# Kernel optimization log

Measured on AMD Instinct MI355X. Metric: run time of the kernel, lower is better.

Reference implementation:

```python
import jax, jax.numpy as jnp
import numpy as np

T, B, L, D = 32, 128, 1024, 256  # timesteps, batch, memory slots, word_vec_size(=rnn_size)


def setup_inputs() -> dict:
    key = jax.random.key(0)
    ks = jax.random.split(key, 20)
    f = lambda k, s: jax.random.normal(k, s, dtype=jnp.float32) * 0.05
    return {
        "emb_utts": f(ks[0], (T, B, D)),
        "hr0": f(ks[1], (B, D)),
        "cr0": f(ks[2], (B, D)),
        "hw0": f(ks[3], (B, D)),
        "cw0": f(ks[4], (B, D)),
        "M": f(ks[5], (B, L, D)),
        "mask": jax.random.randint(ks[6], (B, L), 0, 2).astype(bool),
        "Wih_r": f(ks[7], (4 * D, D)),
        "Whh_r": f(ks[8], (4 * D, D)),
        "bih_r": f(ks[9], (4 * D,)),
        "bhh_r": f(ks[10], (4 * D,)),
        "Wc": f(ks[11], (D, 2 * D)),
        "bc": f(ks[12], (D,)),
        "Wih_w": f(ks[13], (4 * D, D)),
        "Whh_w": f(ks[14], (4 * D, D)),
        "bih_w": f(ks[15], (4 * D,)),
        "bhh_w": f(ks[16], (4 * D,)),
    }


def _lstm_cell(x, h, c, Wih, Whh, bih, bhh):
    # PyTorch LSTMCell gate order: i, f, g, o
    g = x @ Wih.T + h @ Whh.T + bih + bhh
    i, fg, gg, o = jnp.split(g, 4, axis=1)
    i = jax.nn.sigmoid(i)
    fg = jax.nn.sigmoid(fg)
    gg = jnp.tanh(gg)
    o = jax.nn.sigmoid(o)
    c2 = fg * c + i * gg
    return o * jnp.tanh(c2), c2


def reference(emb_utts, hr0, cr0, hw0, cw0, M, mask,
              Wih_r, Whh_r, bih_r, bhh_r, Wc, bc,
              Wih_w, Whh_w, bih_w, bhh_w):
    def step(carry, w):
        hr, cr, hw, cw, Mc = carry
        hr, cr = _lstm_cell(w, hr, cr, Wih_r, Whh_r, bih_r, bhh_r)
        # attention read: z = softmax(masked(hr . M))  -> [B, L]
        z = jnp.einsum('bd,bld->bl', hr, Mc)
        z = jax.nn.softmax(jnp.where(mask, -jnp.inf, z), axis=1)
        m = jnp.einsum('bl,bld->bd', z, Mc)           # gather read [B, D]
        comp = jax.nn.softmax(jnp.concatenate([hr, m], axis=1) @ Wc.T + bc, axis=1)
        hw, cw = _lstm_cell(comp, hw, cw, Wih_w, Whh_w, bih_w, bhh_w)
        # memory rewrite exactly as source: M_new = (1 - z) + hw * z (broadcast)
        Mc = (1.0 - z[:, :, None]) + hw[:, None, :] * z[:, :, None]
        return (hr, cr, hw, cw, Mc), hw

    (hr, cr, hw, cw, M), outputs = jax.lax.scan(
        step, (hr0, cr0, hw0, cw0, M), emb_utts)
    return outputs, hr, cr, hw, cw, M
```

## Files before the change

### kernel.cpp

```cpp
#include <hip/hip_runtime.h>
#include <math.h>

typedef unsigned int u32;
typedef __attribute__((ext_vector_type(2))) _Float16 h2;

#define kT 32
#define OUT_STATES 1048576
#define OUT_M      1179648

union H2U { u32 u; h2 h; };

__device__ __forceinline__ float dot2u(u32 w, u32 x, float acc){
  H2U a; a.u = w; H2U b; b.u = x;
#if __has_builtin(__builtin_amdgcn_fdot2)
  return __builtin_amdgcn_fdot2(a.h, b.h, acc, false);
#else
  acc += (float)a.h.x * (float)b.h.x;
  acc += (float)a.h.y * (float)b.h.y;
  return acc;
#endif
}

__device__ __forceinline__ u32 packf16(float x, float y){
  H2U v; v.h.x = (_Float16)x; v.h.y = (_Float16)y; return v.u;
}

__device__ __forceinline__ u32 alu(const u32* p){
  return __hip_atomic_load((u32*)p, __ATOMIC_RELAXED, __HIP_MEMORY_SCOPE_AGENT);
}
__device__ __forceinline__ float alf(const float* p){
  return __hip_atomic_load((float*)p, __ATOMIC_RELAXED, __HIP_MEMORY_SCOPE_AGENT);
}
__device__ __forceinline__ void asu(u32* p, u32 v){
  __hip_atomic_store(p, v, __ATOMIC_RELAXED, __HIP_MEMORY_SCOPE_AGENT);
}
__device__ __forceinline__ void asf(float* p, float v){
  __hip_atomic_store(p, v, __ATOMIC_RELAXED, __HIP_MEMORY_SCOPE_AGENT);
}

__device__ __forceinline__ void pollk(const u32* f, int n, u32 tgt, int tid){
  if (tid < 64){
    const u32* p = f + ((tid < n) ? tid : 0);
    for (;;){
      if (__all((int)(alu(p) >= tgt))) break;
      __builtin_amdgcn_s_sleep(2);
    }
  }
  __syncthreads();
}

__global__ __launch_bounds__(1024) void k_prep(
        const float* __restrict__ Wih_r, const float* __restrict__ Whh_r,
        const float* __restrict__ bih_r, const float* __restrict__ bhh_r,
        const float* __restrict__ Wc,    const float* __restrict__ bc,
        const float* __restrict__ Wih_w, const float* __restrict__ Whh_w,
        const float* __restrict__ bih_w, const float* __restrict__ bhh_w,
        const unsigned char* __restrict__ maskraw,
        u32* WAp, u32* WEp, u32* Wcp, float* bA, float* bE, float* bcf,
        float* wcs, unsigned char* mbuf, u32* flags){
  __shared__ int sb[3];
  if (threadIdx.x < 3) sb[threadIdx.x] = 0;
  __syncthreads();
  if (threadIdx.x < 512){
    unsigned char c = maskraw[threadIdx.x];
    if (c > 1u) atomicOr(&sb[0], 1);
    if ((threadIdx.x & 3) != 0 && c != 0) atomicOr(&sb[1], 1);
    if ((threadIdx.x & 3) == 1 && c == 0x3F) atomicOr(&sb[2], 1);
  }
  __syncthreads();
  int mode = (!sb[0]) ? (sb[1] ? 1 : 0) : (sb[2] ? 2 : 3);

  int idx = blockIdx.x * 1024 + threadIdx.x;
  if (idx < 262144){
    int kp = idx >> 10, col = idx & 1023;
    int k0 = 2 * kp;
    float v0 = (k0 < 256) ? Wih_r[col * 256 + k0] : Whh_r[col * 256 + k0 - 256];
    float v1 = (k0 + 1 < 256) ? Wih_r[col * 256 + k0 + 1]
                              : Whh_r[col * 256 + k0 + 1 - 256];
    WAp[idx] = packf16(v0, v1);
  } else if (idx < 524288){
    int i = idx - 262144;
    int kp = i >> 10, col = i & 1023;
    int k0 = 2 * kp;
    float v0 = (k0 < 256) ? Wih_w[col * 256 + k0] : Whh_w[col * 256 + k0 - 256];
    float v1 = (k0 + 1 < 256) ? Wih_w[col * 256 + k0 + 1]
                              : Whh_w[col * 256 + k0 + 1 - 256];
    WEp[i] = packf16(v0, v1);
  } else if (idx < 589824){
    int i = idx - 524288;
    int kp = i >> 8, col = i & 255;
    int k0 = 2 * kp;
    Wcp[i] = packf16(Wc[col * 512 + k0], Wc[col * 512 + k0 + 1]);
  } else if (idx < 590848){
    int i = idx - 589824;
    bA[i] = bih_r[i] + bhh_r[i];
  } else if (idx < 591872){
    int i = idx - 590848;
    bE[i] = bih_w[i] + bhh_w[i];
  } else if (idx < 592128){
    int i = idx - 591872;
    bcf[i] = bc[i];
  } else if (idx < 592384){
    int c = idx - 592128;
    float s = 0.f;
    for (int k = 0; k < 256; k++) s += Wc[c * 512 + 256 + k];
    wcs[c] = s;
  } else if (idx < 723456){
    int l = idx - 592384;
    unsigned char mv;
    if      (mode == 0) mv = (((const int*)maskraw)[l] != 0);
    else if (mode == 1) mv = (maskraw[l] != 0);
    else if (mode == 2) mv = ((maskraw[2*l] | maskraw[2*l+1]) != 0);
    else                mv = (((const unsigned int*)maskraw)[l] != 0);
    mbuf[l] = mv;
  } else if (idx < 724032){
    flags[idx - 723456] = 0;
  }
}

__global__ __launch_bounds__(1024) void k_pre(
        const float* __restrict__ emb, const u32* __restrict__ WAp,
        u32* __restrict__ gxp){
  __shared__ u32 wt[16384];
  __shared__ u32 xt[128 * 129];
  int t = blockIdx.x, c0 = blockIdx.y * 128, tid = threadIdx.x;
  for (int i = 0; i < 16; i++){
    int idx = i * 1024 + tid;
    wt[idx] = WAp[(size_t)(idx >> 7) * 1024 + c0 + (idx & 127)];
    int b = idx >> 7, kp = idx & 127;
    float2 e2 = *(const float2*)(emb + (size_t)t * 32768 + b * 256 + 2 * kp);
    xt[b * 129 + kp] = packf16(e2.x, e2.y);
  }
  __syncthreads();
  int b = tid & 127, cg = tid >> 7;
  float acc[16];
  #pragma unroll
  for (int j = 0; j < 16; j++) acc[j] = 0.f;
  const u32* xrow = xt + b * 129;
  for (int kp = 0; kp < 128; kp++){
    u32 xv = xrow[kp];
    const uint4* wr = (const uint4*)(wt + kp * 128 + cg * 16);
    #pragma unroll
    for (int j4 = 0; j4 < 4; j4++){
      uint4 wv = wr[j4];
      acc[4*j4+0] = dot2u(wv.x, xv, acc[4*j4+0]);
      acc[4*j4+1] = dot2u(wv.y, xv, acc[4*j4+1]);
      acc[4*j4+2] = dot2u(wv.z, xv, acc[4*j4+2]);
      acc[4*j4+3] = dot2u(wv.w, xv, acc[4*j4+3]);
    }
  }
  u32* gp = gxp + ((size_t)t * 128 + b) * 512 + (c0 >> 1) + cg * 8;
  #pragma unroll
  for (int i = 0; i < 8; i++) gp[i] = packf16(acc[2*i], acc[2*i+1]);
}

__device__ __forceinline__ void gemv256(const u32* __restrict__ W,
        const u32* xh, float* psum, int tid){
  int cg = tid & 255, ks = tid >> 8;
  const uint4* wp = (const uint4*)W + (size_t)ks * 32 * 256 + cg;
  const u32* xk = xh + ks * 32;
  float a0 = 0.f, a1 = 0.f, a2 = 0.f, a3 = 0.f;
  #pragma unroll 8
  for (int i = 0; i < 32; i++){
    uint4 wv = wp[(size_t)i * 256];
    u32 xp = xk[i];
    a0 = dot2u(wv.x, xp, a0);  a1 = dot2u(wv.y, xp, a1);
    a2 = dot2u(wv.z, xp, a2);  a3 = dot2u(wv.w, xp, a3);
  }
  float4 r; r.x = a0; r.y = a1; r.z = a2; r.w = a3;
  *(float4*)&psum[ks * 1024 + cg * 4] = r;
}

__device__ __forceinline__ void gemv128x256(const u32* __restrict__ W,
        const u32* xh, float* psum, int tid){
  int c = tid & 255, ks = tid >> 8;
  const u32* wp = W + (size_t)(ks * 32) * 256 + c;
  const u32* xk = xh + ks * 32;
  float a = 0.f;
  #pragma unroll 8
  for (int i = 0; i < 32; i++) a = dot2u(wp[(size_t)i * 256], xk[i], a);
  psum[ks * 256 + c] = a;
}

__device__ void scan_half(int k, const float* __restrict__ M0,
        const unsigned char* __restrict__ mbuf, const float* __restrict__ hrf,
        float* spbuf, float* mpbuf, float* msbuf, u32* fT0, const u32* fR,
        char* sc, int tid){
  float* ps   = (float*)(sc);
  float* wred = (float*)(sc + 16640);
  float* sred = (float*)(sc + 16704);
  float* hr0l = (float*)(sc + 16768);
  int row = k >> 1, half = k & 1;
  pollk(fR + row, 1, 1u, tid);
  if (tid < 256) hr0l[tid] = alf(hrf + row * 256 + tid);
  __syncthreads();
  int w = tid >> 6, lane = tid & 63;
  float4 hrv = *(const float4*)&hr0l[lane * 4];
  float run_max = -INFINITY, S = 0.f;
  float m0 = 0.f, m1 = 0.f, m2 = 0.f, m3 = 0.f;
  int l0 = half * 512 + w * 32;
  for (int l = l0; l < l0 + 32; ++l){
    float4 Mv = *(const float4*)(M0 + ((size_t)row * 1024 + l) * 256 + lane * 4);
    float part = Mv.x * hrv.x + Mv.y * hrv.y + Mv.z * hrv.z + Mv.w * hrv.w;
    #pragma unroll
    for (int mm = 32; mm >= 1; mm >>= 1) part += __shfl_xor(part, mm, 64);
    float s = mbuf[row * 1024 + l] ? -INFINITY : part;
    if (lane == 0) asf(spbuf + row * 1024 + l, s);
    float nm = fmaxf(run_max, s);
    if (nm > -INFINITY){
      float sc2 = expf(run_max - nm);
      float p   = expf(s - nm);
      S = S * sc2 + p;
      m0 = m0 * sc2 + p * Mv.x;  m1 = m1 * sc2 + p * Mv.y;
      m2 = m2 * sc2 + p * Mv.z;  m3 = m3 * sc2 + p * Mv.w;
      run_max = nm;
    }
  }
  if (lane == 0){ wred[w] = run_max; sred[w] = S; }
  ps[w * 260 + lane * 4 + 0] = m0;
  ps[w * 260 + lane * 4 + 1] = m1;
  ps[w * 260 + lane * 4 + 2] = m2;
  ps[w * 260 + lane * 4 + 3] = m3;
  __syncthreads();
  float gmax = -INFINITY;
  #pragma unroll
  for (int w2 = 0; w2 < 16; w2++) gmax = fmaxf(gmax, wred[w2]);
  float Sg = 0.f;
  #pragma unroll
  for (int w2 = 0; w2 < 16; w2++) Sg += sred[w2] * expf(wred[w2] - gmax);
  if (tid < 256){
    float mv = 0.f;
    #pragma unroll
    for (int w2 = 0; w2 < 16; w2++) mv += ps[w2 * 260 + tid] * expf(wred[w2] - gmax);
    asf(mpbuf + k * 256 + tid, mv);
  }
  if (tid == 0){ asf(msbuf + 2 * k, gmax); asf(msbuf + 2 * k + 1, Sg); }
  __syncthreads();
  if (tid == 0) asu(fT0 + k, 1u);
}

__global__ __launch_bounds__(1024, 4) void k_main(
        const float* __restrict__ hr0, const float* __restrict__ cr0,
        const float* __restrict__ hw0, const float* __restrict__ cw0,
        const float* __restrict__ M0,
        const u32* __restrict__ WAp, const u32* __restrict__ WEp,
        const u32* __restrict__ Wcp, const float* __restrict__ bA,
        const float* __restrict__ bE, const float* __restrict__ bcf,
        const float* __restrict__ wcs, const unsigned char* __restrict__ mbuf,
        const u32* __restrict__ gxp,
        float* __restrict__ hrf, float* __restrict__ ubuf,
        float* __restrict__ vcbuf, float* __restrict__ gwbuf,
        u32* __restrict__ hwp, float* __restrict__ zsbuf,
        float* __restrict__ hwfin, float* __restrict__ spbuf,
        float* __restrict__ mpbuf, float* __restrict__ msbuf,
        u32* __restrict__ flags, float* __restrict__ out){
  __shared__ __attribute__((aligned(16))) char smem[86016];
  int bid = blockIdx.x, tid = threadIdx.x;
  int w = tid >> 6, lane = tid & 63;
  u32* fR  = flags;
  u32* fGv = flags + 128;
  u32* fG  = flags + 192;
  u32* fW  = flags + 256;
  u32* fT0 = flags + 320;

  if (bid < 128){
    int b = bid;
    float* psum = (float*)(smem);
    u32*  xh    = (u32*)(smem + 16384);
    float* hr_f = (float*)(smem + 16896);
    const u32* WRh = WAp + 128 * 1024;
    float cst = (tid < 256) ? cr0[b * 256 + tid] : 0.f;
    if (tid < 128){
      float2 h0 = *(const float2*)(hr0 + b * 256 + 2 * tid);
      xh[tid] = packf16(h0.x, h0.y);
    }
    __syncthreads();
    for (int t = 0; t < kT; t++){
      if (t >= 2) pollk(fW + (b >> 1), 1, (u32)(t - 1), tid);
      u32 gx0 = 0, gx1 = 0, gx2 = 0, gx3 = 0;
      if (tid < 256){
        const u32* gx = gxp + ((size_t)t * 128 + b) * 512;
        gx0 = gx[tid >> 1];          gx1 = gx[128 + (tid >> 1)];
        gx2 = gx[256 + (tid >> 1)];  gx3 = gx[384 + (tid >> 1)];
      }
      gemv256(WRh, xh, psum, tid);
      __syncthreads();
      if (tid < 256){
        H2U p0, p1, p2, p3;
        p0.u = gx0; p1.u = gx1; p2.u = gx2; p3.u = gx3;
        int hi = tid & 1;
        float gi = (hi ? (float)p0.h.y : (float)p0.h.x) + bA[tid];
        float gf = (hi ? (float)p1.h.y : (float)p1.h.x) + bA[256 + tid];
        float gg = (hi ? (float)p2.h.y : (float)p2.h.x) + bA[512 + tid];
        float go = (hi ? (float)p3.h.y : (float)p3.h.x) + bA[768 + tid];
        #pragma unroll
        for (int ks = 0; ks < 4; ks++){
          gi += psum[ks * 1024 + tid];
          gf += psum[ks * 1024 + 256 + tid];
          gg += psum[ks * 1024 + 512 + tid];
          go += psum[ks * 1024 + 768 + tid];
        }
        float i_ = 1.f / (1.f + expf(-gi));
        float f_ = 1.f / (1.f + expf(-gf));
        float g_ = tanhf(gg);
        float o_ = 1.f / (1.f + expf(-go));
        float c2 = f_ * cst + i_ * g_;
        cst = c2;
        float h = o_ * tanhf(c2);
        hr_f[tid] = h;
        asf(hrf + (t & 1) * 32768 + b * 256 + tid, h);
        if (t == kT - 1){
          out[OUT_STATES          + b * 256 + tid] = h;
          out[OUT_STATES +  32768 + b * 256 + tid] = c2;
        }
      }
      __syncthreads();
      if (tid < 128) xh[tid] = packf16(hr_f[2 * tid], hr_f[2 * tid + 1]);
      __syncthreads();
      gemv128x256(Wcp, xh, psum, tid);
      __syncthreads();
      if (tid < 256){
        float u = psum[tid] + psum[256 + tid] + psum[512 + tid] + psum[768 + tid];
        asf(ubuf + (t & 1) * 32768 + b * 256 + tid, u);
      }
      __syncthreads();
      if (tid == 0) asu(fR + b, (u32)(t + 1));
      if (t == 0)
        scan_half(bid, M0, mbuf, hrf, spbuf, mpbuf, msbuf, fT0, fR,
                  smem + 49152, tid);
    }
  } else if (bid < 192){
    int g = bid - 128, r0 = 2 * g, r1 = 2 * g + 1;
    float* psum = (float*)(smem);
    u32*  xh    = (u32*)(smem + 32768);
    for (int t = 0; t < kT; t++){
      if (t == 0){
        if (tid < 128){
          float2 h0 = *(const float2*)(hw0 + r0 * 256 + 2 * tid);
          xh[tid] = packf16(h0.x, h0.y);
        } else if (tid < 256){
          int j = tid - 128;
          float2 h0 = *(const float2*)(hw0 + r1 * 256 + 2 * j);
          xh[tid] = packf16(h0.x, h0.y);
        }
      } else {
        pollk(fW + g, 1, (u32)t, tid);
        if (tid < 128)
          xh[tid] = alu(hwp + ((t - 1) & 1) * 16384 + r0 * 128 + tid);
        else if (tid < 256)
          xh[tid] = alu(hwp + ((t - 1) & 1) * 16384 + r1 * 128 + (tid - 128));
      }
      __syncthreads();
      {
        int c = tid & 255, ks = tid >> 8;
        const u32* wp = Wcp + 32768 + (size_t)(ks * 32) * 256 + c;
        const u32* x0 = xh + ks * 32;
        const u32* x1 = xh + 128 + ks * 32;
        float a0 = 0.f, a1 = 0.f;
        #pragma unroll 8
        for (int ii = 0; ii < 32; ii++){
          u32 wv = wp[(size_t)ii * 256];
          a0 = dot2u(wv, x0[ii], a0);
          a1 = dot2u(wv, x1[ii], a1);
        }
        psum[ks * 512 + c] = a0;
        psum[ks * 512 + 256 + c] = a1;
      }
      __syncthreads();
      if (tid < 512){
        int rr = tid >> 8, c = tid & 255;
        float v = psum[rr * 256 + c] + psum[512 + rr * 256 + c]
                + psum[1024 + rr * 256 + c] + psum[1536 + rr * 256 + c];
        asf(vcbuf + (t & 1) * 32768 + (2 * g + rr) * 256 + c, v);
      }
      __syncthreads();
      if (tid == 0) asu(fGv + g, (u32)(t + 1));
      {
        int cg = tid & 255, ks = tid >> 8;
        const uint4* wp = (const uint4*)(WEp + 128 * 1024)
                        + (size_t)(ks * 32) * 256 + cg;
        const u32* x0 = xh + ks * 32;
        const u32* x1 = xh + 128 + ks * 32;
        float a0=0.f,a1=0.f,a2=0.f,a3=0.f,b0=0.f,b1=0.f,b2=0.f,b3=0.f;
        #pragma unroll 4
        for (int ii = 0; ii < 32; ii++){
          uint4 wv = wp[(size_t)ii * 256];
          u32 xp0 = x0[ii], xp1 = x1[ii];
          a0 = dot2u(wv.x, xp0, a0);  a1 = dot2u(wv.y, xp0, a1);
          a2 = dot2u(wv.z, xp0, a2);  a3 = dot2u(wv.w, xp0, a3);
          b0 = dot2u(wv.x, xp1, b0);  b1 = dot2u(wv.y, xp1, b1);
          b2 = dot2u(wv.z, xp1, b2);  b3 = dot2u(wv.w, xp1, b3);
        }
        float4 ra; ra.x=a0; ra.y=a1; ra.z=a2; ra.w=a3;
        float4 rb; rb.x=b0; rb.y=b1; rb.z=b2; rb.w=b3;
        *(float4*)&psum[ks * 1024 + cg * 4] = ra;
        *(float4*)&psum[4096 + ks * 1024 + cg * 4] = rb;
      }
      __syncthreads();
      #pragma unroll
      for (int rr = 0; rr < 2; rr++){
        float v = psum[rr * 4096 + tid] + psum[rr * 4096 + 1024 + tid]
                + psum[rr * 4096 + 2048 + tid] + psum[rr * 4096 + 3072 + tid];
        asf(gwbuf + (t & 1) * 131072 + (2 * g + rr) * 1024 + tid, v);
      }
      __syncthreads();
      if (tid == 0) asu(fG + g, (u32)(t + 1));
      if (t == 0)
        scan_half(bid, M0, mbuf, hrf, spbuf, mpbuf, msbuf, fT0, fR,
                  smem + 49152, tid);
    }
  } else {
    int g = bid - 192, r0g = 2 * g;
    float* psum  = (float*)(smem);
    u32*  xh    = (u32*)(smem + 32768);
    float* comp  = (float*)(smem + 33792);
    float* hw_f  = (float*)(smem + 35840);
    float* m_f   = (float*)(smem + 37888);
    float* wcs_l = (float*)(smem + 39936);
    float* bc_l  = (float*)(smem + 40960);
    float* redA  = (float*)(smem + 41984);
    float* redB  = (float*)(smem + 42048);
    float* redC  = (float*)(smem + 42112);
    float* redD  = (float*)(smem + 42176);
    float* bE_l  = (float*)(smem + 43008);
    int row = tid >> 9, i = tid & 511;
    int brow = r0g + row;
    if (tid < 256){ wcs_l[tid] = wcs[tid]; bc_l[tid] = bcf[tid]; }
    bE_l[tid] = bE[tid];
    float cst = 0.f;
    if (i < 256){
      hw_f[row * 256 + i] = hw0[brow * 256 + i];
      cst = cw0[brow * 256 + i];
    }
    unsigned char mkA = mbuf[brow * 1024 + i];
    unsigned char mkB = mbuf[brow * 1024 + 512 + i];
    float zA = 0.f, zB = 0.f;
    __syncthreads();
    scan_half(bid, M0, mbuf, hrf, spbuf, mpbuf, msbuf, fT0, fR,
              smem + 49152, tid);

    for (int t = 0; t < kT; t++){
      pollk(fR + r0g, 2, (u32)(t + 1), tid);
      float hrv = 0.f, ureg = 0.f;
      if (i < 256){
        hrv  = alf(hrf + (t & 1) * 32768 + brow * 256 + i);
        ureg = alf(ubuf + (t & 1) * 32768 + brow * 256 + i);
      }
      float e = -INFINITY;
      if (t == 0){
        pollk(fT0 + 4 * g, 4, 1u, tid);
        int kA2 = 2 * brow, kB2 = 2 * brow + 1;
        float maxA = alf(msbuf + 2 * kA2), SAv = alf(msbuf + 2 * kA2 + 1);
        float maxB = alf(msbuf + 2 * kB2), SBv = alf(msbuf + 2 * kB2 + 1);
        float Gm = fmaxf(maxA, maxB);
        float eAc = expf(maxA - Gm), eBc = expf(maxB - Gm);
        float Sg = SAv * eAc + SBv * eBc;
        zA = expf(alf(spbuf + brow * 1024 + i) - Gm) / Sg;
        zB = expf(alf(spbuf + brow * 1024 + 512 + i) - Gm) / Sg;
        if (i < 256){
          float mv = (alf(mpbuf + kA2 * 256 + i) * eAc
                    + alf(mpbuf + kB2 * 256 + i) * eBc) / Sg;
          m_f[row * 256 + i] = mv;
        }
        __syncthreads();
        if (i < 128)
          xh[row * 128 + i] = packf16(m_f[row * 256 + 2 * i],
                                      m_f[row * 256 + 2 * i + 1]);
        __syncthreads();
        {
          int c = tid & 255, ks = tid >> 8;
          const u32* wp = Wcp + 32768 + (size_t)(ks * 32) * 256 + c;
          const u32* x0 = xh + ks * 32;
          const u32* x1 = xh + 128 + ks * 32;
          float a0 = 0.f, a1 = 0.f;
          #pragma unroll 8
          for (int ii = 0; ii < 32; ii++){
            u32 wv = wp[(size_t)ii * 256];
            a0 = dot2u(wv, x0[ii], a0);
            a1 = dot2u(wv, x1[ii], a1);
          }
          psum[ks * 512 + c] = a0;
          psum[ks * 512 + 256 + c] = a1;
        }
        __syncthreads();
        if (i < 256){
          float vcm = psum[row * 256 + i] + psum[512 + row * 256 + i]
                    + psum[1024 + row * 256 + i] + psum[1536 + row * 256 + i];
          e = ureg + vcm + bc_l[i];
        }
      } else {
        float v1 = (i < 256) ? hrv : 0.f;
        float v2 = (i < 256) ? hrv * hw_f[row * 256 + i] : 0.f;
        #pragma unroll
        for (int mm = 32; mm >= 1; mm >>= 1){
          v1 += __shfl_xor(v1, mm, 64);  v2 += __shfl_xor(v2, mm, 64);
        }
        if (lane == 0){ redA[w] = v1; redB[w] = v2; }
        __syncthreads();
        float S1 = 0.f, S2 = 0.f;
        #pragma unroll
        for (int k2 = 0; k2 < 8; k2++){
          S1 += redA[row * 8 + k2];  S2 += redB[row * 8 + k2];
        }
        float sA = mkA ? -INFINITY : (1.f - zA) * S1 + zA * S2;
        float sB = mkB ? -INFINITY : (1.f - zB) * S1 + zB * S2;
        float mx = fmaxf(sA, sB);
        #pragma unroll
        for (int mm = 32; mm >= 1; mm >>= 1) mx = fmaxf(mx, __shfl_xor(mx, mm, 64));
        if (lane == 0) redC[w] = mx;
        __syncthreads();
        float gm = -INFINITY;
        #pragma unroll
        for (int k2 = 0; k2 < 8; k2++) gm = fmaxf(gm, redC[row * 8 + k2]);
        float pA_ = expf(sA - gm), pB_ = expf(sB - gm);
        float ps = pA_ + pB_;
        #pragma unroll
        for (int mm = 32; mm >= 1; mm >>= 1) ps += __shfl_xor(ps, mm, 64);
        if (lane == 0) redD[w] = ps;
        __syncthreads();
        float Ss = 0.f;
        #pragma unroll
        for (int k2 = 0; k2 < 8; k2++) Ss += redD[row * 8 + k2];
        float znA = pA_ / Ss, znB = pB_ / Ss;
        float a1 = znA * (1.f - zA) + znB * (1.f - zB);
        float a2 = znA * zA + znB * zB;
        #pragma unroll
        for (int mm = 32; mm >= 1; mm >>= 1){
          a1 += __shfl_xor(a1, mm, 64);  a2 += __shfl_xor(a2, mm, 64);
        }
        if (lane == 0){ redA[w] = a1; redB[w] = a2; }
        __syncthreads();
        float Ab = 0.f, Cb = 0.f;
        #pragma unroll
        for (int k2 = 0; k2 < 8; k2++){
          Ab += redA[row * 8 + k2];  Cb += redB[row * 8 + k2];
        }
        zA = znA;  zB = znB;
        pollk(fGv + g, 1, (u32)(t + 1), tid);
        if (i < 256){
          float vc = alf(vcbuf + (t & 1) * 32768 + brow * 256 + i);
          e = ureg + Ab * wcs_l[i] + Cb * vc + bc_l[i];
        }
      }
      float ev = (i < 256) ? e : -INFINITY;
      float mx2 = ev;
      #pragma unroll
      for (int mm = 32; mm >= 1; mm >>= 1) mx2 = fmaxf(mx2, __shfl_xor(mx2, mm, 64));
      if (lane == 0) redC[w] = mx2;
      __syncthreads();
      float emax = -INFINITY;
      #pragma unroll
      for (int k2 = 0; k2 < 8; k2++) emax = fmaxf(emax, redC[row * 8 + k2]);
      float pe = (i < 256) ? expf(ev - emax) : 0.f;
      float ps2 = pe;
      #pragma unroll
      for (int mm = 32; mm >= 1; mm >>= 1) ps2 += __shfl_xor(ps2, mm, 64);
      if (lane == 0) redD[w] = ps2;
      if (i < 256) comp[row * 256 + i] = pe;
      __syncthreads();
      float esum = 0.f;
      #pragma unroll
      for (int k2 = 0; k2 < 8; k2++) esum += redD[row * 8 + k2];
      if (i < 128)
        xh[row * 128 + i] = packf16(comp[row * 256 + 2 * i],
                                    comp[row * 256 + 2 * i + 1]);
      __syncthreads();
      {
        int cg = tid & 255, ks = tid >> 8;
        const uint4* wp = (const uint4*)WEp + (size_t)(ks * 32) * 256 + cg;
        const u32* x0 = xh + ks * 32;
        const u32* x1 = xh + 128 + ks * 32;
        float a0=0.f,a1=0.f,a2=0.f,a3=0.f,b0=0.f,b1=0.f,b2=0.f,b3=0.f;
        #pragma unroll 4
        for (int ii = 0; ii < 32; ii++){
          uint4 wv = wp[(size_t)ii * 256];
          u32 xp0 = x0[ii], xp1 = x1[ii];
          a0 = dot2u(wv.x, xp0, a0);  a1 = dot2u(wv.y, xp0, a1);
          a2 = dot2u(wv.z, xp0, a2);  a3 = dot2u(wv.w, xp0, a3);
          b0 = dot2u(wv.x, xp1, b0);  b1 = dot2u(wv.y, xp1, b1);
          b2 = dot2u(wv.z, xp1, b2);  b3 = dot2u(wv.w, xp1, b3);
        }
        float4 ra; ra.x=a0; ra.y=a1; ra.z=a2; ra.w=a3;
        float4 rb; rb.x=b0; rb.y=b1; rb.z=b2; rb.w=b3;
        *(float4*)&psum[ks * 1024 + cg * 4] = ra;
        *(float4*)&psum[4096 + ks * 1024 + cg * 4] = rb;
      }
      __syncthreads();
      pollk(fG + g, 1, (u32)(t + 1), tid);
      if (i < 256){
        float rinv = 1.f / esum;
        const float* gwp = gwbuf + (t & 1) * 131072 + brow * 1024;
        float si = psum[row*4096 + i]        + psum[row*4096 + 1024 + i]
                 + psum[row*4096 + 2048 + i] + psum[row*4096 + 3072 + i];
        float sf = psum[row*4096 + 256 + i]  + psum[row*4096 + 1280 + i]
                 + psum[row*4096 + 2304 + i] + psum[row*4096 + 3328 + i];
        float sg2= psum[row*4096 + 512 + i]  + psum[row*4096 + 1536 + i]
                 + psum[row*4096 + 2560 + i] + psum[row*4096 + 3584 + i];
        float so = psum[row*4096 + 768 + i]  + psum[row*4096 + 1792 + i]
                 + psum[row*4096 + 2816 + i] + psum[row*4096 + 3840 + i];
        float gi = bE_l[i]       + alf(gwp + i)       + si  * rinv;
        float gf = bE_l[256 + i] + alf(gwp + 256 + i) + sf  * rinv;
        float gg = bE_l[512 + i] + alf(gwp + 512 + i) + sg2 * rinv;
        float go = bE_l[768 + i] + alf(gwp + 768 + i) + so  * rinv;
        float i_ = 1.f / (1.f + expf(-gi));
        float f_ = 1.f / (1.f + expf(-gf));
        float g_ = tanhf(gg);
        float o_ = 1.f / (1.f + expf(-go));
        float c2 = f_ * cst + i_ * g_;
        cst = c2;
        float h = o_ * tanhf(c2);
        hw_f[row * 256 + i] = h;
        out[(size_t)t * 32768 + brow * 256 + i] = h;
        if (t == kT - 1){
          out[OUT_STATES + 65536 + brow * 256 + i] = h;
          out[OUT_STATES + 98304 + brow * 256 + i] = c2;
        }
      }
      __syncthreads();
      if (i < 128)
        asu(hwp + (t & 1) * 16384 + brow * 128 + i,
            packf16(hw_f[row * 256 + 2 * i], hw_f[row * 256 + 2 * i + 1]));
      __syncthreads();
      if (tid == 0) asu(fW + g, (u32)(t + 1));
    }
    if (i < 256) asf(hwfin + brow * 256 + i, hw_f[row * 256 + i]);
    asf(zsbuf + brow * 1024 + i, zA);
    asf(zsbuf + brow * 1024 + 512 + i, zB);
    __syncthreads();
    if (tid == 0) asu(fW + g, (u32)(kT + 1));
  }

  {
    int mrow = bid >> 1, half = bid & 1;
    pollk(fW + (mrow >> 1), 1, (u32)(kT + 1), tid);
    float* zl  = (float*)(smem + 49152);
    float* hwl = (float*)(smem + 51200);
    if (tid < 512) zl[tid] = alf(zsbuf + mrow * 1024 + half * 512 + tid);
    else if (tid < 768) hwl[tid - 512] = alf(hwfin + mrow * 256 + (tid - 512));
    __syncthreads();
    float* Mout = out + OUT_M + (size_t)mrow * 262144 + (size_t)half * 131072;
    for (int it = 0; it < 32; it++){
      int idx = it * 1024 + tid;
      int l = idx >> 6, d4 = (idx & 63) << 2;
      float z = zl[l], omz = 1.f - z;
      float4 h4 = *(const float4*)&hwl[d4];
      float4 v;
      v.x = omz + h4.x * z;  v.y = omz + h4.y * z;
      v.z = omz + h4.z * z;  v.w = omz + h4.w * z;
      *(float4*)(Mout + (size_t)l * 256 + d4) = v;
    }
  }
}

extern "C" void kernel_launch(void* const* d_in, const int* in_sizes, int n_in,
                              void* d_out, int out_size, void* d_ws, size_t ws_size,
                              hipStream_t stream){
  const float* emb   = (const float*)d_in[0];
  const float* hr0   = (const float*)d_in[1];
  const float* cr0   = (const float*)d_in[2];
  const float* hw0   = (const float*)d_in[3];
  const float* cw0   = (const float*)d_in[4];
  const float* M0    = (const float*)d_in[5];
  const unsigned char* maskraw = (const unsigned char*)d_in[6];
  const float* Wih_r = (const float*)d_in[7];
  const float* Whh_r = (const float*)d_in[8];
  const float* bih_r = (const float*)d_in[9];
  const float* bhh_r = (const float*)d_in[10];
  const float* Wc    = (const float*)d_in[11];
  const float* bc    = (const float*)d_in[12];
  const float* Wih_w = (const float*)d_in[13];
  const float* Whh_w = (const float*)d_in[14];
  const float* bih_w = (const float*)d_in[15];
  const float* bhh_w = (const float*)d_in[16];
  float* out = (float*)d_out;

  char* ws = (char*)d_ws;
  u32*  WAp   = (u32*)(ws);
  u32*  WEp   = (u32*)(ws + 1048576);
  u32*  Wcp   = (u32*)(ws + 2097152);
  float* bA   = (float*)(ws + 2359296);
  float* bE   = (float*)(ws + 2363392);
  float* bcf  = (float*)(ws + 2367488);
  float* wcs  = (float*)(ws + 2368512);
  unsigned char* mbuf = (unsigned char*)(ws + 2369536);
  u32*  flags = (u32*)(ws + 2500608);
  float* hrf  = (float*)(ws + 2504704);
  float* ubuf = (float*)(ws + 2766848);
  float* vcbuf= (float*)(ws + 3028992);
  float* gwbuf= (float*)(ws + 3291136);
  u32*  hwp   = (u32*)(ws + 4339712);
  float* zsbuf= (float*)(ws + 4470784);
  float* hwfin= (float*)(ws + 4995072);
  float* spbuf= (float*)(ws + 5126144);
  float* mpbuf= (float*)(ws + 5650432);
  float* msbuf= (float*)(ws + 5912576);
  u32*  gxp   = (u32*)(ws + 5914624);

  k_prep<<<dim3(708), dim3(1024), 0, stream>>>(
      Wih_r, Whh_r, bih_r, bhh_r, Wc, bc, Wih_w, Whh_w, bih_w, bhh_w,
      maskraw, WAp, WEp, Wcp, bA, bE, bcf, wcs, mbuf, flags);
  k_pre<<<dim3(32, 8), dim3(1024), 0, stream>>>(emb, WAp, gxp);
  k_main<<<dim3(256), dim3(1024), 0, stream>>>(
      hr0, cr0, hw0, cw0, M0, WAp, WEp, Wcp, bA, bE, bcf, wcs, mbuf, gxp,
      hrf, ubuf, vcbuf, gwbuf, hwp, zsbuf, hwfin, spbuf, mpbuf, msbuf,
      flags, out);
}
```

Baseline: 645.1 us.

## Compute Wc·hw partial locally in writer block, dropping cross-block vc flag handoff

The projection of hw through the second half of Wc was computed by one group of blocks and handed to another through a global buffer plus a flag poll. It is now computed inside the block that produces hw, right after the LSTM update, and kept in a register for the next step. This removes one cross-block flag, a global round trip and a poll from the critical recurrent path, but adds that small matvec and extra barriers to the writer block's serial chain. The prep kernel's weight repacking is also reindexed so reads are coalesced instead of writes, and a wider flag range is zeroed.

```diff
diff --git a/kernel.cpp b/kernel.cpp
--- a/kernel.cpp
+++ b/kernel.cpp
@@ -72,25 +72,24 @@
 
   int idx = blockIdx.x * 1024 + threadIdx.x;
   if (idx < 262144){
-    int kp = idx >> 10, col = idx & 1023;
+    int col = idx >> 8, kp = idx & 255;
     int k0 = 2 * kp;
     float v0 = (k0 < 256) ? Wih_r[col * 256 + k0] : Whh_r[col * 256 + k0 - 256];
-    float v1 = (k0 + 1 < 256) ? Wih_r[col * 256 + k0 + 1]
-                              : Whh_r[col * 256 + k0 + 1 - 256];
-    WAp[idx] = packf16(v0, v1);
+    float v1 = (k0 < 256) ? Wih_r[col * 256 + k0 + 1]
+                          : Whh_r[col * 256 + k0 + 1 - 256];
+    WAp[kp * 1024 + col] = packf16(v0, v1);
   } else if (idx < 524288){
     int i = idx - 262144;
-    int kp = i >> 10, col = i & 1023;
+    int col = i >> 8, kp = i & 255;
     int k0 = 2 * kp;
     float v0 = (k0 < 256) ? Wih_w[col * 256 + k0] : Whh_w[col * 256 + k0 - 256];
-    float v1 = (k0 + 1 < 256) ? Wih_w[col * 256 + k0 + 1]
-                              : Whh_w[col * 256 + k0 + 1 - 256];
-    WEp[i] = packf16(v0, v1);
+    float v1 = (k0 < 256) ? Wih_w[col * 256 + k0 + 1]
+                          : Whh_w[col * 256 + k0 + 1 - 256];
+    WEp[kp * 1024 + col] = packf16(v0, v1);
   } else if (idx < 589824){
     int i = idx - 524288;
-    int kp = i >> 8, col = i & 255;
-    int k0 = 2 * kp;
-    Wcp[i] = packf16(Wc[col * 512 + k0], Wc[col * 512 + k0 + 1]);
+    int col = i >> 8, kp = i & 255;
+    Wcp[kp * 256 + col] = packf16(Wc[col * 512 + 2 * kp], Wc[col * 512 + 2 * kp + 1]);
   } else if (idx < 590848){
     int i = idx - 589824;
     bA[i] = bih_r[i] + bhh_r[i];
@@ -113,7 +112,7 @@
     else if (mode == 2) mv = ((maskraw[2*l] | maskraw[2*l+1]) != 0);
     else                mv = (((const unsigned int*)maskraw)[l] != 0);
     mbuf[l] = mv;
-  } else if (idx < 724032){
+  } else if (idx < 724224){
     flags[idx - 723456] = 0;
   }
 }
@@ -249,7 +248,7 @@
         const float* __restrict__ wcs, const unsigned char* __restrict__ mbuf,
         const u32* __restrict__ gxp,
         float* __restrict__ hrf, float* __restrict__ ubuf,
-        float* __restrict__ vcbuf, float* __restrict__ gwbuf,
+        float* __restrict__ gwbuf,
         u32* __restrict__ hwp, float* __restrict__ zsbuf,
         float* __restrict__ hwfin, float* __restrict__ spbuf,
         float* __restrict__ mpbuf, float* __restrict__ msbuf,
@@ -258,7 +257,6 @@
   int bid = blockIdx.x, tid = threadIdx.x;
   int w = tid >> 6, lane = tid & 63;
   u32* fR  = flags;
-  u32* fGv = flags + 128;
   u32* fG  = flags + 192;
   u32* fW  = flags + 256;
   u32* fT0 = flags + 320;
@@ -351,30 +349,6 @@
           xh[tid] = alu(hwp + ((t - 1) & 1) * 16384 + r1 * 128 + (tid - 128));
       }
       __syncthreads();
-      {
-        int c = tid & 255, ks = tid >> 8;
-        const u32* wp = Wcp + 32768 + (size_t)(ks * 32) * 256 + c;
-        const u32* x0 = xh + ks * 32;
-        const u32* x1 = xh + 128 + ks * 32;
-        float a0 = 0.f, a1 = 0.f;
-        #pragma unroll 8
-        for (int ii = 0; ii < 32; ii++){
-          u32 wv = wp[(size_t)ii * 256];
-          a0 = dot2u(wv, x0[ii], a0);
-          a1 = dot2u(wv, x1[ii], a1);
-        }
-        psum[ks * 512 + c] = a0;
-        psum[ks * 512 + 256 + c] = a1;
-      }
-      __syncthreads();
-      if (tid < 512){
-        int rr = tid >> 8, c = tid & 255;
-        float v = psum[rr * 256 + c] + psum[512 + rr * 256 + c]
-                + psum[1024 + rr * 256 + c] + psum[1536 + rr * 256 + c];
-        asf(vcbuf + (t & 1) * 32768 + (2 * g + rr) * 256 + c, v);
-      }
-      __syncthreads();
-      if (tid == 0) asu(fGv + g, (u32)(t + 1));
       {
         int cg = tid & 255, ks = tid >> 8;
         const uint4* wp = (const uint4*)(WEp + 128 * 1024)
@@ -434,7 +408,7 @@
     }
     unsigned char mkA = mbuf[brow * 1024 + i];
     unsigned char mkB = mbuf[brow * 1024 + 512 + i];
-    float zA = 0.f, zB = 0.f;
+    float zA = 0.f, zB = 0.f, vcreg = 0.f;
     __syncthreads();
     scan_half(bid, M0, mbuf, hrf, spbuf, mpbuf, msbuf, fT0, fR,
               smem + 49152, tid);
@@ -536,11 +510,8 @@
           Ab += redA[row * 8 + k2];  Cb += redB[row * 8 + k2];
         }
         zA = znA;  zB = znB;
-        pollk(fGv + g, 1, (u32)(t + 1), tid);
-        if (i < 256){
-          float vc = alf(vcbuf + (t & 1) * 32768 + brow * 256 + i);
-          e = ureg + Ab * wcs_l[i] + Cb * vc + bc_l[i];
-        }
+        if (i < 256)
+          e = ureg + Ab * wcs_l[i] + Cb * vcreg + bc_l[i];
       }
       float ev = (i < 256) ? e : -INFINITY;
       float mx2 = ev;
@@ -622,6 +593,32 @@
             packf16(hw_f[row * 256 + 2 * i], hw_f[row * 256 + 2 * i + 1]));
       __syncthreads();
       if (tid == 0) asu(fW + g, (u32)(t + 1));
+      if (t < kT - 1){
+        if (i < 128)
+          xh[row * 128 + i] = packf16(hw_f[row * 256 + 2 * i],
+                                      hw_f[row * 256 + 2 * i + 1]);
+        __syncthreads();
+        {
+          int c = tid & 255, ks = tid >> 8;
+          const u32* wp = Wcp + 32768 + (size_t)(ks * 32) * 256 + c;
+          const u32* x0 = xh + ks * 32;
+          const u32* x1 = xh + 128 + ks * 32;
+          float a0 = 0.f, a1 = 0.f;
+          #pragma unroll 8
+          for (int ii = 0; ii < 32; ii++){
+            u32 wv = wp[(size_t)ii * 256];
+            a0 = dot2u(wv, x0[ii], a0);
+            a1 = dot2u(wv, x1[ii], a1);
+          }
+          psum[ks * 512 + c] = a0;
+          psum[ks * 512 + 256 + c] = a1;
+        }
+        __syncthreads();
+        if (i < 256)
+          vcreg = psum[row * 256 + i] + psum[512 + row * 256 + i]
+                + psum[1024 + row * 256 + i] + psum[1536 + row * 256 + i];
+        __syncthreads();
+      }
     }
     if (i < 256) asf(hwfin + brow * 256 + i, hw_f[row * 256 + i]);
     asf(zsbuf + brow * 1024 + i, zA);
@@ -686,7 +683,6 @@
   u32*  flags = (u32*)(ws + 2500608);
   float* hrf  = (float*)(ws + 2504704);
   float* ubuf = (float*)(ws + 2766848);
-  float* vcbuf= (float*)(ws + 3028992);
   float* gwbuf= (float*)(ws + 3291136);
   u32*  hwp   = (u32*)(ws + 4339712);
   float* zsbuf= (float*)(ws + 4470784);
@@ -702,6 +698,6 @@
   k_pre<<<dim3(32, 8), dim3(1024), 0, stream>>>(emb, WAp, gxp);
   k_main<<<dim3(256), dim3(1024), 0, stream>>>(
       hr0, cr0, hw0, cw0, M0, WAp, WEp, Wcp, bA, bE, bcf, wcs, mbuf, gxp,
-      hrf, ubuf, vcbuf, gwbuf, hwp, zsbuf, hwfin, spbuf, mpbuf, msbuf,
+      hrf, ubuf, gwbuf, hwp, zsbuf, hwfin, spbuf, mpbuf, msbuf,
       flags, out);
 }
```

Measured after the change: 682.0 us. 1.06x slower.
